# Kernel tuning notes

Hardware: AMD Instinct MI355X
Metric: run time of the kernel (lower is better)

Reference implementation:

```python
import jax, jax.numpy as jnp
import numpy as np

B, N, D_IN, D_OUT, E = 16, 16384, 128, 128, 65536
LN_EPS = 1e-5


def setup_inputs() -> dict:
    key = jax.random.key(0)
    k1, k2, k3, k4 = jax.random.split(key, 4)
    x = jax.random.normal(k1, (B, N, D_IN), dtype=jnp.float32)
    edge_index = jax.random.randint(k2, (2, E), 0, N, dtype=jnp.int64)
    W_self = jax.random.normal(k3, (D_OUT, D_IN), dtype=jnp.float32) / np.sqrt(D_IN)
    W_neigh = jax.random.normal(k4, (D_OUT, D_IN), dtype=jnp.float32) / np.sqrt(D_IN)
    return {
        "x": x,
        "edge_index": edge_index,
        "batch_size": B,
        "W_self": W_self,
        "W_neigh": W_neigh,
        "bias": jnp.zeros((D_OUT,), jnp.float32),
        "gamma": jnp.ones((D_OUT,), jnp.float32),
        "beta": jnp.zeros((D_OUT,), jnp.float32),
    }


def reference(x, edge_index, batch_size, W_self, W_neigh, bias, gamma, beta):
    b, n, d = x.shape
    src, dst = edge_index[0], edge_index[1]
    # expand edge index for disjoint batched graphs: add per-graph node offsets
    offsets = (jnp.arange(batch_size, dtype=src.dtype) * n)[:, None]  # [B,1]
    src_e = (src[None, :] + offsets).reshape(-1)  # [B*E]
    dst_e = (dst[None, :] + offsets).reshape(-1)
    x_flat = x.reshape(batch_size * n, d)
    # scatter-sum neighbor features and degrees, then mean
    agg = jax.ops.segment_sum(x_flat[src_e], dst_e, num_segments=batch_size * n)
    deg = jax.ops.segment_sum(jnp.ones_like(dst_e, dtype=x_flat.dtype), dst_e,
                              num_segments=batch_size * n)
    neigh = agg / jnp.maximum(deg, 1.0)[:, None]
    out = x_flat @ W_self.T + neigh @ W_neigh.T + bias  # [B*N, D_OUT]
    # LayerNorm over last dim
    mu = jnp.mean(out, axis=-1, keepdims=True)
    var = jnp.mean(jnp.square(out - mu), axis=-1, keepdims=True)
    out = (out - mu) * jax.lax.rsqrt(var + LN_EPS) * gamma + beta
    out = jax.nn.relu(out)
    return out.reshape(batch_size, n, -1)
```

## Files before the change

kernel.cpp:

```cpp
#include <hip/hip_runtime.h>
#include <hip/hip_bf16.h>
#include <hip/hip_fp16.h>
#include <stdint.h>

#define B_ 16
#define N_ 16384
#define D_ 128
#define E_ 65536

typedef __attribute__((ext_vector_type(8))) __bf16 bf16x8;
typedef __attribute__((ext_vector_type(4))) float f32x4;
typedef __attribute__((ext_vector_type(8))) _Float16 half8;

__device__ __forceinline__ uint16_t f2bf(float f) {
    union { float f; uint32_t u; } v;
    v.f = f;
    uint32_t u = v.u;
    uint32_t r = (u + 0x7fffu + ((u >> 16) & 1u)) >> 16;
    return (uint16_t)r;
}

__device__ __forceinline__ int As_off(int ch, int l16) {
    int c = (ch & 7) ^ ((l16 >> 4) & 1);
    return ch * 1024 + ((l16 ^ c) << 4);
}

__device__ __forceinline__ bool ei_is64(const int* __restrict__ ei, int t) {
    int w = ei[2 * (t & 63) + 1];
    return __ballot(w != 0) == 0ull;
}

__device__ __forceinline__ void conv_chunk(const float* __restrict__ x,
                                           _Float16* __restrict__ xh,
                                           int g, int t) {
    size_t base = (size_t)g * 8192 + (size_t)t * 8;
#pragma unroll
    for (int it = 0; it < 4; it++) {
        size_t idx = base + (size_t)it * 2048;
        const float4* p = (const float4*)(x + idx);
        float4 v0 = p[0], v1 = p[1];
        union { _Float16 hh[8]; uint4 u; } pk;
        pk.hh[0] = (_Float16)v0.x; pk.hh[1] = (_Float16)v0.y;
        pk.hh[2] = (_Float16)v0.z; pk.hh[3] = (_Float16)v0.w;
        pk.hh[4] = (_Float16)v1.x; pk.hh[5] = (_Float16)v1.y;
        pk.hh[6] = (_Float16)v1.z; pk.hh[7] = (_Float16)v1.w;
        *(uint4*)(xh + idx) = pk.u;
    }
}

__global__ void k_a(const int* __restrict__ ei,
                    const float* __restrict__ wself,
                    const float* __restrict__ wneigh,
                    const float* __restrict__ x,
                    int* __restrict__ deg,
                    uint16_t* __restrict__ wpack,
                    _Float16* __restrict__ xh) {
    int t = threadIdx.x;
    int bid = blockIdx.x;
    if (bid < 256) {
        bool is64 = ei_is64(ei, t);
        int e = bid * 256 + t;
        int d = is64 ? ei[2 * (E_ + e)] : ei[E_ + e];
        atomicAdd(&deg[d], 1);
    } else if (bid < 384) {
        int g = (bid - 256) * 256 + t;
        int j = g & 7;
        int lane = (g >> 3) & 63;
        int nt = (g >> 9) & 7;
        int ks = g >> 12;
        int k = ks * 32 + (lane >> 4) * 8 + j;
        int n = nt * 16 + (lane & 15);
        float v = (k < 128) ? wself[n * 128 + k] : wneigh[n * 128 + (k - 128)];
        wpack[g] = f2bf(v);
    } else {
        conv_chunk(x, xh, bid - 384, t);
    }
}

__global__ void k_scan(const int* __restrict__ deg, int* __restrict__ off,
                       int* __restrict__ cur) {
    __shared__ int ps[256];
    int t = threadIdx.x;
    int vals[64];
    const int4* dv = (const int4*)(deg + t * 64);
    int s = 0;
#pragma unroll
    for (int i = 0; i < 16; i++) {
        int4 v = dv[i];
        vals[4 * i + 0] = v.x; vals[4 * i + 1] = v.y;
        vals[4 * i + 2] = v.z; vals[4 * i + 3] = v.w;
        s += v.x + v.y + v.z + v.w;
    }
    ps[t] = s;
    __syncthreads();
#pragma unroll
    for (int st = 1; st < 256; st <<= 1) {
        int add = (t >= st) ? ps[t - st] : 0;
        __syncthreads();
        ps[t] += add;
        __syncthreads();
    }
    int run = ps[t] - s;
#pragma unroll
    for (int i = 0; i < 64; i++) {
        off[t * 64 + i] = run;
        cur[t * 64 + i] = run;
        run += vals[i];
    }
    if (t == 255) off[N_] = run;
}

__global__ void k_b(const int* __restrict__ ei, const float* __restrict__ x,
                    int* __restrict__ cur, int* __restrict__ adj,
                    _Float16* __restrict__ xh, int do_conv) {
    int t = threadIdx.x;
    int bid = blockIdx.x;
    if (bid < 256) {
        bool is64 = ei_is64(ei, t);
        int e = bid * 256 + t;
        int s = is64 ? ei[2 * e] : ei[e];
        int d = is64 ? ei[2 * (E_ + e)] : ei[E_ + e];
        int p = atomicAdd(&cur[d], 1);
        adj[p] = s;
    } else if (do_conv) {
        conv_chunk(x, xh, 1024 + (bid - 256), t);
    }
}

template <bool USE_H>
__global__ __launch_bounds__(256, 8) void k_main(
    const float* __restrict__ x,
    const _Float16* __restrict__ xh,
    const int* __restrict__ off,
    const int* __restrict__ adj,
    const uint16_t* __restrict__ wpack,
    const float* __restrict__ bias,
    const float* __restrict__ gamma_,
    const float* __restrict__ beta_,
    float* __restrict__ out) {
    __shared__ __align__(16) unsigned char smem[16896];
    __shared__ float prm[3][128];
    unsigned char* Asb = smem;
    float* Cs = (float*)smem;

    int t = threadIdx.x;
    int bid = blockIdx.x;
    int xcd = bid & 7;
    int w = bid >> 12;
    int tile = (bid >> 3) & 511;
    int b = w * 8 + xcd;
    int node0 = tile * 32;

    if (t < 128) {
        prm[0][t] = bias[t];
        prm[1][t] = gamma_[t];
        prm[2][t] = beta_[t];
    }

    int hw = t >> 5, l = t & 31;
    int p = l >> 4;
    int dl = l & 15;

    int obase = node0 + hw * 4;
    int oo[5];
#pragma unroll
    for (int i = 0; i < 5; i++) oo[i] = off[obase + i];

    const _Float16* xgb = xh + (size_t)b * N_ * D_;
    const float* xgf = x + (size_t)b * N_ * D_;

#pragma unroll
    for (int i = 0; i < 2; i++) {
        int r2 = hw * 4 + i * 2 + p;
        int nd = node0 + r2;
        float f[8];
        if (USE_H) {
            uint4 raw = *(const uint4*)(xgb + (size_t)nd * D_ + dl * 8);
            half8 hv = __builtin_bit_cast(half8, raw);
#pragma unroll
            for (int j = 0; j < 8; j++) f[j] = (float)hv[j];
        } else {
            const float4* pv = (const float4*)(xgf + (size_t)nd * D_ + dl * 8);
            float4 a0 = pv[0], a1 = pv[1];
            f[0] = a0.x; f[1] = a0.y; f[2] = a0.z; f[3] = a0.w;
            f[4] = a1.x; f[5] = a1.y; f[6] = a1.z; f[7] = a1.w;
        }
        uint32_t pk[4];
#pragma unroll
        for (int j = 0; j < 4; j++)
            pk[j] = (uint32_t)f2bf(f[2 * j]) | ((uint32_t)f2bf(f[2 * j + 1]) << 16);
        int ks = dl >> 2, qd = dl & 3;
        int mt2 = r2 >> 4, m2 = r2 & 15;
        *(uint4*)(Asb + As_off(ks * 2 + mt2, qd * 16 + m2)) =
            make_uint4(pk[0], pk[1], pk[2], pk[3]);
    }

#pragma unroll
    for (int i = 0; i < 4; i++) {
        int r2 = hw * 4 + i;
        int o0 = oo[i], o1 = oo[i + 1];
        float a[8];
        if (USE_H) {
            __half2 hacc[4];
#pragma unroll
            for (int j = 0; j < 4; j++) hacc[j] = __float2half2_rn(0.f);
            union { uint4 u; __half2 h[4]; } c0, c1;
            int e = o0 + p;
            for (; e + 2 < o1; e += 4) {
                int s0 = adj[e], s1 = adj[e + 2];
                c0.u = *(const uint4*)(xgb + (size_t)s0 * D_ + dl * 8);
                c1.u = *(const uint4*)(xgb + (size_t)s1 * D_ + dl * 8);
#pragma unroll
                for (int j = 0; j < 4; j++) hacc[j] = __hadd2(hacc[j], c0.h[j]);
#pragma unroll
                for (int j = 0; j < 4; j++) hacc[j] = __hadd2(hacc[j], c1.h[j]);
            }
            if (e < o1) {
                int s0 = adj[e];
                c0.u = *(const uint4*)(xgb + (size_t)s0 * D_ + dl * 8);
#pragma unroll
                for (int j = 0; j < 4; j++) hacc[j] = __hadd2(hacc[j], c0.h[j]);
            }
#pragma unroll
            for (int j = 0; j < 4; j++) {
                float2 fj = __half22float2(hacc[j]);
                a[2 * j] = fj.x;
                a[2 * j + 1] = fj.y;
            }
        } else {
#pragma unroll
            for (int j = 0; j < 8; j++) a[j] = 0.f;
            for (int e = o0 + p; e < o1; e += 2) {
                int s0 = adj[e];
                const float4* pv = (const float4*)(xgf + (size_t)s0 * D_ + dl * 8);
                float4 v0 = pv[0], v1 = pv[1];
                a[0] += v0.x; a[1] += v0.y; a[2] += v0.z; a[3] += v0.w;
                a[4] += v1.x; a[5] += v1.y; a[6] += v1.z; a[7] += v1.w;
            }
        }
#pragma unroll
        for (int j = 0; j < 8; j++) a[j] += __shfl_xor(a[j], 16, 64);
        if (p == 0) {
            float sc = 1.f / fmaxf((float)(o1 - o0), 1.f);
            uint32_t pk[4];
#pragma unroll
            for (int j = 0; j < 4; j++)
                pk[j] = (uint32_t)f2bf(a[2 * j] * sc) |
                        ((uint32_t)f2bf(a[2 * j + 1] * sc) << 16);
            int kc = 16 + dl;
            int ks = kc >> 2, qd = kc & 3;
            int mt2 = r2 >> 4, m2 = r2 & 15;
            *(uint4*)(Asb + As_off(ks * 2 + mt2, qd * 16 + m2)) =
                make_uint4(pk[0], pk[1], pk[2], pk[3]);
        }
    }

    __syncthreads();

    int wv = t >> 6;
    int lane = t & 63;
    f32x4 accv[2][2];
#pragma unroll
    for (int i = 0; i < 2; i++)
#pragma unroll
        for (int j = 0; j < 2; j++) {
            f32x4 z = {0.f, 0.f, 0.f, 0.f};
            accv[i][j] = z;
        }

    const uint4* wp = (const uint4*)wpack;
#pragma unroll
    for (int ks = 0; ks < 8; ks++) {
        uint4 b0u = wp[(ks * 8 + 2 * wv + 0) * 64 + lane];
        uint4 b1u = wp[(ks * 8 + 2 * wv + 1) * 64 + lane];
        bf16x8 bf0 = __builtin_bit_cast(bf16x8, b0u);
        bf16x8 bf1 = __builtin_bit_cast(bf16x8, b1u);
#pragma unroll
        for (int mtt = 0; mtt < 2; mtt++) {
            bf16x8 a = *(const bf16x8*)(Asb + As_off(ks * 2 + mtt, lane));
            accv[mtt][0] = __builtin_amdgcn_mfma_f32_16x16x32_bf16(a, bf0, accv[mtt][0], 0, 0, 0);
            accv[mtt][1] = __builtin_amdgcn_mfma_f32_16x16x32_bf16(a, bf1, accv[mtt][1], 0, 0, 0);
        }
    }

    __syncthreads();

#pragma unroll
    for (int mtt = 0; mtt < 2; mtt++)
#pragma unroll
        for (int ntl = 0; ntl < 2; ntl++)
#pragma unroll
            for (int rg = 0; rg < 4; rg++) {
                int row = mtt * 16 + (lane >> 4) * 4 + rg;
                int col = (2 * wv + ntl) * 16 + (lane & 15);
                Cs[row * 132 + (col >> 5) * 33 + (col & 31)] = accv[mtt][ntl][rg];
            }

    __syncthreads();

    {
        int r = t >> 3;
        int h = t & 7;
        int node = node0 + r;
        const size_t xrow = ((size_t)b * N_ + node) * D_;
        int cbase = r * 132 + (h >> 1) * 33 + (h & 1) * 16;
        float s1 = 0.f, s2 = 0.f;
#pragma unroll
        for (int i = 0; i < 16; i++) {
            float v = Cs[cbase + i] + prm[0][h * 16 + i];
            s1 += v;
            s2 += v * v;
        }
        s1 += __shfl_xor(s1, 1, 64);
        s2 += __shfl_xor(s2, 1, 64);
        s1 += __shfl_xor(s1, 2, 64);
        s2 += __shfl_xor(s2, 2, 64);
        s1 += __shfl_xor(s1, 4, 64);
        s2 += __shfl_xor(s2, 4, 64);
        float mu = s1 * (1.f / 128.f);
        float var = s2 * (1.f / 128.f) - mu * mu;
        float rstd = rsqrtf(var + 1e-5f);

        float* orow = out + xrow;
#pragma unroll
        for (int c = 0; c < 4; c++) {
            float4 o;
            float tmp[4];
#pragma unroll
            for (int j = 0; j < 4; j++) {
                int i0 = c * 4 + j;
                int d0 = h * 16 + i0;
                float v = Cs[cbase + i0] + prm[0][d0];
                tmp[j] = fmaxf((v - mu) * rstd * prm[1][d0] + prm[2][d0], 0.f);
            }
            o.x = tmp[0]; o.y = tmp[1]; o.z = tmp[2]; o.w = tmp[3];
            *(float4*)&orow[h * 16 + c * 4] = o;
        }
    }
}

extern "C" void kernel_launch(void* const* d_in, const int* in_sizes, int n_in,
                              void* d_out, int out_size, void* d_ws, size_t ws_size,
                              hipStream_t stream) {
    (void)in_sizes; (void)n_in; (void)out_size;
    const float* x      = (const float*)d_in[0];
    const int*   ei     = (const int*)d_in[1];
    const float* wself  = (const float*)d_in[3];
    const float* wneigh = (const float*)d_in[4];
    const float* bias   = (const float*)d_in[5];
    const float* gma    = (const float*)d_in[6];
    const float* bta    = (const float*)d_in[7];
    float* out = (float*)d_out;

    char* ws = (char*)d_ws;
    int* deg        = (int*)(ws);
    int* off        = (int*)(ws + 65536);
    int* cur        = (int*)(ws + 131584);
    int* adj        = (int*)(ws + 197120);
    uint16_t* wpack = (uint16_t*)(ws + 459264);
    _Float16* xh    = (_Float16*)(ws + 524800);

    bool use_h = d_ws != nullptr &&
                 ws_size >= (size_t)524800 + (size_t)B_ * N_ * D_ * 2;

    hipMemsetAsync(deg, 0, N_ * sizeof(int), stream);
    k_a<<<use_h ? 1408 : 384, 256, 0, stream>>>(ei, wself, wneigh, x, deg,
                                                wpack, xh);
    k_scan<<<1, 256, 0, stream>>>(deg, off, cur);
    k_b<<<use_h ? 3328 : 256, 256, 0, stream>>>(ei, x, cur, adj, xh,
                                                use_h ? 1 : 0);
    if (use_h)
        k_main<true><<<B_ * (N_ / 32), 256, 0, stream>>>(x, xh, off, adj, wpack,
                                                         bias, gma, bta, out);
    else
        k_main<false><<<B_ * (N_ / 32), 256, 0, stream>>>(x, xh, off, adj, wpack,
                                                          bias, gma, bta, out);
}
```

Baseline: 330.5 us.

## Switch GEMM operands from bf16 to fp16 and rebalance conversion across kernels

Replaces the bf16 MFMA with the fp16 MFMA. The fp16 copy of x is now written straight into shared memory without a float round-trip and bf16 repacking. The neighbor-sum reduction across half-waves and the mean scaling stay in packed half2 arithmetic, and weights are packed as fp16. It also moves more of the x-to-fp16 conversion work from k_b into k_a by changing the grid sizes, to balance the two pre-kernels. This cuts per-element conversion ALU in the main kernel, at the cost of fp16 range and precision in the mean reduction.

```diff
diff --git a/kernel.cpp b/kernel.cpp
--- a/kernel.cpp
+++ b/kernel.cpp
@@ -8,17 +8,8 @@
 #define D_ 128
 #define E_ 65536
 
-typedef __attribute__((ext_vector_type(8))) __bf16 bf16x8;
+typedef __attribute__((ext_vector_type(8))) _Float16 half8;
 typedef __attribute__((ext_vector_type(4))) float f32x4;
-typedef __attribute__((ext_vector_type(8))) _Float16 half8;
-
-__device__ __forceinline__ uint16_t f2bf(float f) {
-    union { float f; uint32_t u; } v;
-    v.f = f;
-    uint32_t u = v.u;
-    uint32_t r = (u + 0x7fffu + ((u >> 16) & 1u)) >> 16;
-    return (uint16_t)r;
-}
 
 __device__ __forceinline__ int As_off(int ch, int l16) {
     int c = (ch & 7) ^ ((l16 >> 4) & 1);
@@ -71,7 +62,9 @@
         int k = ks * 32 + (lane >> 4) * 8 + j;
         int n = nt * 16 + (lane & 15);
         float v = (k < 128) ? wself[n * 128 + k] : wneigh[n * 128 + (k - 128)];
-        wpack[g] = f2bf(v);
+        union { _Float16 h; uint16_t u; } cv;
+        cv.h = (_Float16)v;
+        wpack[g] = cv.u;
     } else {
         conv_chunk(x, xh, bid - 384, t);
     }
@@ -123,7 +116,7 @@
         int p = atomicAdd(&cur[d], 1);
         adj[p] = s;
     } else if (do_conv) {
-        conv_chunk(x, xh, 1024 + (bid - 256), t);
+        conv_chunk(x, xh, 2048 + (bid - 256), t);
     }
 }
 
@@ -173,33 +166,29 @@
     for (int i = 0; i < 2; i++) {
         int r2 = hw * 4 + i * 2 + p;
         int nd = node0 + r2;
-        float f[8];
+        uint4 raw;
         if (USE_H) {
-            uint4 raw = *(const uint4*)(xgb + (size_t)nd * D_ + dl * 8);
-            half8 hv = __builtin_bit_cast(half8, raw);
-#pragma unroll
-            for (int j = 0; j < 8; j++) f[j] = (float)hv[j];
+            raw = *(const uint4*)(xgb + (size_t)nd * D_ + dl * 8);
         } else {
             const float4* pv = (const float4*)(xgf + (size_t)nd * D_ + dl * 8);
             float4 a0 = pv[0], a1 = pv[1];
-            f[0] = a0.x; f[1] = a0.y; f[2] = a0.z; f[3] = a0.w;
-            f[4] = a1.x; f[5] = a1.y; f[6] = a1.z; f[7] = a1.w;
-        }
-        uint32_t pk[4];
-#pragma unroll
-        for (int j = 0; j < 4; j++)
-            pk[j] = (uint32_t)f2bf(f[2 * j]) | ((uint32_t)f2bf(f[2 * j + 1]) << 16);
+            union { _Float16 hh[8]; uint4 u; } cv;
+            cv.hh[0] = (_Float16)a0.x; cv.hh[1] = (_Float16)a0.y;
+            cv.hh[2] = (_Float16)a0.z; cv.hh[3] = (_Float16)a0.w;
+            cv.hh[4] = (_Float16)a1.x; cv.hh[5] = (_Float16)a1.y;
+            cv.hh[6] = (_Float16)a1.z; cv.hh[7] = (_Float16)a1.w;
+            raw = cv.u;
+        }
         int ks = dl >> 2, qd = dl & 3;
         int mt2 = r2 >> 4, m2 = r2 & 15;
-        *(uint4*)(Asb + As_off(ks * 2 + mt2, qd * 16 + m2)) =
-            make_uint4(pk[0], pk[1], pk[2], pk[3]);
+        *(uint4*)(Asb + As_off(ks * 2 + mt2, qd * 16 + m2)) = raw;
     }
 
 #pragma unroll
     for (int i = 0; i < 4; i++) {
         int r2 = hw * 4 + i;
         int o0 = oo[i], o1 = oo[i + 1];
-        float a[8];
+        uint32_t pk[4];
         if (USE_H) {
             __half2 hacc[4];
 #pragma unroll
@@ -223,11 +212,19 @@
             }
 #pragma unroll
             for (int j = 0; j < 4; j++) {
-                float2 fj = __half22float2(hacc[j]);
-                a[2 * j] = fj.x;
-                a[2 * j + 1] = fj.y;
+                int wbits = __builtin_bit_cast(int, hacc[j]);
+                int obits = __shfl_xor(wbits, 16, 64);
+                hacc[j] = __hadd2(hacc[j], __builtin_bit_cast(__half2, obits));
+            }
+            float scf = 1.f / fmaxf((float)(o1 - o0), 1.f);
+            __half2 sc2 = __float2half2_rn(scf);
+#pragma unroll
+            for (int j = 0; j < 4; j++) {
+                __half2 rr = __hmul2(hacc[j], sc2);
+                pk[j] = __builtin_bit_cast(uint32_t, rr);
             }
         } else {
+            float a[8];
 #pragma unroll
             for (int j = 0; j < 8; j++) a[j] = 0.f;
             for (int e = o0 + p; e < o1; e += 2) {
@@ -237,16 +234,18 @@
                 a[0] += v0.x; a[1] += v0.y; a[2] += v0.z; a[3] += v0.w;
                 a[4] += v1.x; a[5] += v1.y; a[6] += v1.z; a[7] += v1.w;
             }
-        }
-#pragma unroll
-        for (int j = 0; j < 8; j++) a[j] += __shfl_xor(a[j], 16, 64);
+#pragma unroll
+            for (int j = 0; j < 8; j++) a[j] += __shfl_xor(a[j], 16, 64);
+            float scf = 1.f / fmaxf((float)(o1 - o0), 1.f);
+#pragma unroll
+            for (int j = 0; j < 4; j++) {
+                union { _Float16 hh[2]; uint32_t u; } cv;
+                cv.hh[0] = (_Float16)(a[2 * j] * scf);
+                cv.hh[1] = (_Float16)(a[2 * j + 1] * scf);
+                pk[j] = cv.u;
+            }
+        }
         if (p == 0) {
-            float sc = 1.f / fmaxf((float)(o1 - o0), 1.f);
-            uint32_t pk[4];
-#pragma unroll
-            for (int j = 0; j < 4; j++)
-                pk[j] = (uint32_t)f2bf(a[2 * j] * sc) |
-                        ((uint32_t)f2bf(a[2 * j + 1] * sc) << 16);
             int kc = 16 + dl;
             int ks = kc >> 2, qd = kc & 3;
             int mt2 = r2 >> 4, m2 = r2 & 15;
@@ -273,13 +272,13 @@
     for (int ks = 0; ks < 8; ks++) {
         uint4 b0u = wp[(ks * 8 + 2 * wv + 0) * 64 + lane];
         uint4 b1u = wp[(ks * 8 + 2 * wv + 1) * 64 + lane];
-        bf16x8 bf0 = __builtin_bit_cast(bf16x8, b0u);
-        bf16x8 bf1 = __builtin_bit_cast(bf16x8, b1u);
+        half8 bf0 = __builtin_bit_cast(half8, b0u);
+        half8 bf1 = __builtin_bit_cast(half8, b1u);
 #pragma unroll
         for (int mtt = 0; mtt < 2; mtt++) {
-            bf16x8 a = *(const bf16x8*)(Asb + As_off(ks * 2 + mtt, lane));
-            accv[mtt][0] = __builtin_amdgcn_mfma_f32_16x16x32_bf16(a, bf0, accv[mtt][0], 0, 0, 0);
-            accv[mtt][1] = __builtin_amdgcn_mfma_f32_16x16x32_bf16(a, bf1, accv[mtt][1], 0, 0, 0);
+            half8 a = *(const half8*)(Asb + As_off(ks * 2 + mtt, lane));
+            accv[mtt][0] = __builtin_amdgcn_mfma_f32_16x16x32_f16(a, bf0, accv[mtt][0], 0, 0, 0);
+            accv[mtt][1] = __builtin_amdgcn_mfma_f32_16x16x32_f16(a, bf1, accv[mtt][1], 0, 0, 0);
         }
     }
 
@@ -364,10 +363,10 @@
                  ws_size >= (size_t)524800 + (size_t)B_ * N_ * D_ * 2;
 
     hipMemsetAsync(deg, 0, N_ * sizeof(int), stream);
-    k_a<<<use_h ? 1408 : 384, 256, 0, stream>>>(ei, wself, wneigh, x, deg,
+    k_a<<<use_h ? 2432 : 384, 256, 0, stream>>>(ei, wself, wneigh, x, deg,
                                                 wpack, xh);
     k_scan<<<1, 256, 0, stream>>>(deg, off, cur);
-    k_b<<<use_h ? 3328 : 256, 256, 0, stream>>>(ei, x, cur, adj, xh,
+    k_b<<<use_h ? 2304 : 256, 256, 0, stream>>>(ei, x, cur, adj, xh,
                                                 use_h ? 1 : 0);
     if (use_h)
         k_main<true><<<B_ * (N_ / 32), 256, 0, stream>>>(x, xh, off, adj, wpack,
```

After: 334.1 us. Within noise of the previous version (+1.1%).
